# Performance work log

Measured on AMD Instinct MI355X. Metric: run time of the kernel, lower is better.

The kernel has to match this reference:

```python
import jax, jax.numpy as jnp
import numpy as np
from jax.ops import segment_sum

N_NODES = 50000
N_EDGES = 800000
IN_FEATS = 128
H_FEATS = 256
NUM_CLASSES = 16


def setup_inputs() -> dict:
    key = jax.random.key(0)
    k1, k2, k3, k4, k5 = jax.random.split(key, 5)
    in_feat = jax.random.normal(k1, (N_NODES, IN_FEATS), dtype=jnp.float32)
    src = jax.random.randint(k2, (N_EDGES,), 0, N_NODES, dtype=jnp.int32)
    dst = jax.random.randint(k3, (N_EDGES,), 0, N_NODES, dtype=jnp.int32)
    # Glorot-ish scaled params
    W_gc = jax.random.normal(k4, (IN_FEATS, H_FEATS), dtype=jnp.float32) / np.sqrt(IN_FEATS)
    b_gc = jnp.zeros((H_FEATS,), dtype=jnp.float32)
    W_fc = jax.random.normal(k5, (H_FEATS, NUM_CLASSES), dtype=jnp.float32) / np.sqrt(H_FEATS)
    b_fc = jnp.zeros((NUM_CLASSES,), dtype=jnp.float32)
    return {"in_feat": in_feat, "src": src, "dst": dst,
            "W_gc": W_gc, "b_gc": b_gc, "W_fc": W_fc, "b_fc": b_fc}


def reference(in_feat, src, dst, W_gc, b_gc, W_fc, b_fc):
    n = in_feat.shape[0]
    ones = jnp.ones_like(src, dtype=in_feat.dtype)
    # DGL GraphConv, norm='both': D_out^{-1/2} on source side, sum-aggregate,
    # D_in^{-1/2} on destination side. Degrees clamped to >= 1.
    deg_out = jnp.clip(segment_sum(ones, src, num_segments=n), 1.0)
    deg_in = jnp.clip(segment_sum(ones, dst, num_segments=n), 1.0)
    x = in_feat * jax.lax.rsqrt(deg_out)[:, None]            # [N, in]
    agg = segment_sum(x[src], dst, num_segments=n)           # [N, in] irregular gather+scatter
    agg = agg * jax.lax.rsqrt(deg_in)[:, None]
    # in_feats <= h_feats -> aggregate first, then project (DGL ordering)
    h = agg @ W_gc + b_gc                                    # [N, h]
    h = jax.nn.relu(h)
    logits = h @ W_fc + b_fc                                 # [N, num_classes]
    return jax.nn.sigmoid(logits)
```

## Files before the change

kernel.cpp:

```cpp
#include <hip/hip_runtime.h>
#include <hip/hip_bf16.h>

#define IN_F  128
#define H_F   256
#define NC    16
#define BM    64
#define CAP   64
#define PCAP  8192

typedef short bf16x8 __attribute__((ext_vector_type(8)));
typedef float f32x4  __attribute__((ext_vector_type(4)));

__device__ __forceinline__ unsigned short f2bf(float x) {
    union { float f; unsigned u; } v; v.f = x;
    unsigned r = v.u + 0x7FFF + ((v.u >> 16) & 1);
    return (unsigned short)(r >> 16);
}
__device__ __forceinline__ float bflo(unsigned x) {
    union { unsigned u; float f; } v; v.u = x << 16; return v.f;
}
__device__ __forceinline__ float bfhi(unsigned x) {
    union { unsigned u; float f; } v; v.u = x & 0xffff0000u; return v.f;
}

__global__ void gcn_zero(int* __restrict__ cur, unsigned* __restrict__ xb, int n) {
    int tid = threadIdx.x;
    cur[tid] = 0;
    cur[tid + 256] = 0;
    if (tid < 64) xb[(size_t)n * 64 + tid] = 0;
}

__global__ __launch_bounds__(256) void gcn_part(
    const int* __restrict__ src, const int* __restrict__ dst,
    int* __restrict__ curS, int* __restrict__ curD,
    unsigned short* __restrict__ srcP, unsigned* __restrict__ dstP,
    const float* __restrict__ W_gc, const float* __restrict__ W_fc,
    unsigned short* __restrict__ Wp, unsigned short* __restrict__ Wfp,
    const float* __restrict__ in_feat, unsigned* __restrict__ xb,
    int n_edges, int n_feat4, int nb_edge, int np) {
    __shared__ int cS[256], cD[256];
    int b0 = blockIdx.x, tid = threadIdx.x;
    if (b0 < nb_edge) {
        unsigned sv[16], dv[16];
        int ebase = b0 * 4096;
        #pragma unroll
        for (int r = 0; r < 16; ++r) {
            int e = ebase + r * 256 + tid;
            if (e < n_edges) { sv[r] = (unsigned)src[e]; dv[r] = (unsigned)dst[e]; }
            else { sv[r] = 0xFFFFFFFFu; dv[r] = 0xFFFFFFFFu; }
        }
        cS[tid] = 0; cD[tid] = 0;
        __syncthreads();
        #pragma unroll
        for (int r = 0; r < 16; ++r) {
            if (dv[r] != 0xFFFFFFFFu) {
                atomicAdd(&cS[sv[r] >> 8], 1);
                atomicAdd(&cD[dv[r] >> 8], 1);
            }
        }
        __syncthreads();
        if (tid < np) {
            int c = cS[tid];
            cS[tid] = c ? atomicAdd(&curS[tid], c) : 0;
            c = cD[tid];
            cD[tid] = c ? atomicAdd(&curD[tid], c) : 0;
        }
        __syncthreads();
        #pragma unroll
        for (int r = 0; r < 16; ++r) {
            if (dv[r] != 0xFFFFFFFFu) {
                unsigned s = sv[r], d = dv[r];
                int ps = atomicAdd(&cS[s >> 8], 1);
                if (ps < PCAP) srcP[(size_t)(s >> 8) * PCAP + ps] = (unsigned short)s;
                int pd = atomicAdd(&cD[d >> 8], 1);
                if (pd < PCAP) dstP[(size_t)(d >> 8) * PCAP + pd] =
                    ((d & 255u) << 16) | (s & 0xffffu);
            }
        }
        return;
    }
    int b = b0 - nb_edge;
    if (b < 128) {
        int g = b * 256 + tid;
        {
            int j = g & 7, l = (g >> 3) & 63, t = g >> 9;
            int kt = t & 3, ct = t >> 2;
            int k = kt * 32 + ((l >> 4) << 3) + j;
            int col = ct * 16 + (l & 15);
            Wp[g] = f2bf(W_gc[k * 256 + col]);
        }
        if (g < 4096) {
            int j = g & 7, l = (g >> 3) & 63, kt = g >> 9;
            int k = kt * 32 + ((l >> 4) << 3) + j;
            Wfp[g] = f2bf(W_fc[k * 16 + (l & 15)]);
        }
        return;
    }
    int idx = (b - 128) * 256 + tid;
    if (idx < n_feat4) {
        float4 v = ((const float4*)in_feat)[idx];
        uint2 o;
        o.x = (unsigned)f2bf(v.x) | ((unsigned)f2bf(v.y) << 16);
        o.y = (unsigned)f2bf(v.z) | ((unsigned)f2bf(v.w) << 16);
        ((uint2*)xb)[idx] = o;
    }
}

__global__ __launch_bounds__(256) void gcn_bucket(
    const unsigned short* __restrict__ srcP, const unsigned* __restrict__ dstP,
    const int* __restrict__ curS, const int* __restrict__ curD,
    int* __restrict__ cnt_out, int* __restrict__ cnt_in,
    unsigned short* __restrict__ esrc, unsigned* __restrict__ xb,
    int n, int np) {
    __shared__ unsigned hist[256];
    __shared__ float rr[256];
    __shared__ unsigned short bucket[256 * CAP];
    int p = blockIdx.x, tid = threadIdx.x;
    hist[tid] = 0;
    __syncthreads();
    if (p < np) {
        int cnt = curS[p]; if (cnt > PCAP) cnt = PCAP;
        const unsigned short* sp = srcP + (size_t)p * PCAP;
        for (int i = tid; i < cnt; i += 256)
            atomicAdd(&hist[sp[i] & 255], 1);
        __syncthreads();
        int node = p * 256 + tid;
        if (node < n) cnt_out[node] = (int)hist[tid];
        rr[tid] = rsqrtf(fmaxf((float)hist[tid], 1.0f));
        __syncthreads();
        for (int i = tid; i < 16384; i += 256) {
            int row = i >> 6, el = i & 63;
            int nd = p * 256 + row;
            if (nd < n) {
                unsigned v = xb[(size_t)nd * 64 + el];
                float r = rr[row];
                float lo = bflo(v) * r;
                float hi = bfhi(v) * r;
                xb[(size_t)nd * 64 + el] = (unsigned)f2bf(lo) | ((unsigned)f2bf(hi) << 16);
            }
        }
    } else {
        int pp = p - np;
        unsigned dummy2 = ((unsigned)n & 0xffffu) | (((unsigned)n & 0xffffu) << 16);
        unsigned* bu32 = (unsigned*)bucket;
        for (int i = tid; i < 8192; i += 256) bu32[i] = dummy2;
        int cnt = curD[pp]; if (cnt > PCAP) cnt = PCAP;
        const unsigned* dp = dstP + (size_t)pp * PCAP;
        __syncthreads();
        for (int i = tid; i < cnt; i += 256) {
            unsigned pair = dp[i];
            unsigned dl = pair >> 16;
            unsigned pos = atomicAdd(&hist[dl], 1);
            if (pos < CAP) bucket[(dl << 6) + pos] = (unsigned short)(pair & 0xffffu);
        }
        __syncthreads();
        unsigned* eb = (unsigned*)(esrc + ((size_t)pp << 14));
        const unsigned* bu = (const unsigned*)bucket;
        int maxrow = n - pp * 256;
        int words = (maxrow >= 256) ? 8192 : (maxrow > 0 ? maxrow * 32 : 0);
        for (int i = tid; i < words; i += 256) eb[i] = bu[i];
        int node = pp * 256 + tid;
        if (node < n) cnt_in[node] = (int)hist[tid];
    }
}

__global__ __launch_bounds__(256) void gcn_aggregate(
    const unsigned* __restrict__ xb, const unsigned short* __restrict__ esrc,
    const int* __restrict__ cnt_in, unsigned* __restrict__ aggb, int n) {
    int wave = (blockIdx.x * blockDim.x + threadIdx.x) >> 6;
    int lane = threadIdx.x & 63;
    if (wave >= n) return;
    int wv = __builtin_amdgcn_readfirstlane(wave);
    int cnt = cnt_in[wv];
    if (cnt > CAP) cnt = CAP;
    const unsigned short* es = esrc + ((size_t)wv << 6);
    const uint2* xb2 = (const uint2*)xb;
    int half = lane >> 5;
    int sub  = lane & 31;
    int hsh  = half * 16;
    float a0[8], a1[8], a2[8], a3[8];
    #pragma unroll
    for (int j = 0; j < 8; ++j) { a0[j] = 0.f; a1[j] = 0.f; a2[j] = 0.f; a3[j] = 0.f; }
    for (int i = 0; i < cnt; i += 16) {
        uint4 pa = *(const uint4*)(es + i);
        uint4 pb = *(const uint4*)(es + i + 8);
        unsigned wrd[8];
        wrd[0] = pa.x; wrd[1] = pa.y; wrd[2] = pa.z; wrd[3] = pa.w;
        wrd[4] = pb.x; wrd[5] = pb.y; wrd[6] = pb.z; wrd[7] = pb.w;
        #pragma unroll
        for (int j = 0; j < 8; ++j) {
            int s = (int)((wrd[j] >> hsh) & 0xffffu);
            uint2 v = xb2[(size_t)s * 32 + sub];
            a0[j] += bflo(v.x); a1[j] += bfhi(v.x);
            a2[j] += bflo(v.y); a3[j] += bfhi(v.y);
        }
    }
    float s0 = ((a0[0]+a0[1])+(a0[2]+a0[3]))+((a0[4]+a0[5])+(a0[6]+a0[7]));
    float s1 = ((a1[0]+a1[1])+(a1[2]+a1[3]))+((a1[4]+a1[5])+(a1[6]+a1[7]));
    float s2 = ((a2[0]+a2[1])+(a2[2]+a2[3]))+((a2[4]+a2[5])+(a2[6]+a2[7]));
    float s3 = ((a3[0]+a3[1])+(a3[2]+a3[3]))+((a3[4]+a3[5])+(a3[6]+a3[7]));
    s0 += __shfl_xor(s0, 32);
    s1 += __shfl_xor(s1, 32);
    s2 += __shfl_xor(s2, 32);
    s3 += __shfl_xor(s3, 32);
    if (half == 0) {
        float ri = rsqrtf(fmaxf((float)cnt, 1.0f));
        uint2 o;
        o.x = (unsigned)f2bf(s0 * ri) | ((unsigned)f2bf(s1 * ri) << 16);
        o.y = (unsigned)f2bf(s2 * ri) | ((unsigned)f2bf(s3 * ri) << 16);
        ((uint2*)aggb)[(size_t)wv * 32 + sub] = o;
    }
}

__global__ __launch_bounds__(256) void gcn_mlp(
    const unsigned* __restrict__ aggb, const unsigned short* __restrict__ Wp,
    const unsigned short* __restrict__ Wfp, const float* __restrict__ b_gc,
    const float* __restrict__ b_fc, float* __restrict__ out, int n) {
    extern __shared__ char smraw[];
    unsigned short* Wl  = (unsigned short*)smraw;
    unsigned short* Wfl = Wl + 32768;
    unsigned short* Al  = Wfl + 4096;
    unsigned short* Hl  = Al + 8192;
    float* bgl = (float*)(Hl + 16384);
    float* bfl = bgl + 256;

    int tid = threadIdx.x;
    int lane = tid & 63, w = tid >> 6;

    for (int i = tid; i < 4096; i += 256) ((float4*)Wl)[i]  = ((const float4*)Wp)[i];
    for (int i = tid; i < 512;  i += 256) ((float4*)Wfl)[i] = ((const float4*)Wfp)[i];
    bgl[tid] = b_gc[tid];
    if (tid < NC) bfl[tid] = b_fc[tid];

    int ntiles = (n + BM - 1) / BM;
    for (int tile = blockIdx.x; tile < ntiles; tile += gridDim.x) {
        __syncthreads();
        int row0 = tile * BM;
        for (int i = tid; i < 1024; i += 256) {
            int r = i >> 4, cb = i & 15;
            int node = row0 + r;
            float4 v = (node < n) ? ((const float4*)aggb)[(size_t)node * 16 + cb]
                                  : make_float4(0.f, 0.f, 0.f, 0.f);
            ((float4*)Al)[r * 16 + (cb ^ (r & 7))] = v;
        }
        __syncthreads();

        bf16x8 af[4];
        {
            int r = lane & 15;
            #pragma unroll
            for (int kt = 0; kt < 4; ++kt) {
                int cb = kt * 4 + (lane >> 4);
                af[kt] = *((const bf16x8*)Al + ((w * 16 + r) * 16 + (cb ^ (r & 7))));
            }
        }
        f32x4 acc[16];
        #pragma unroll
        for (int ct = 0; ct < 16; ++ct) {
            acc[ct] = (f32x4){0.f, 0.f, 0.f, 0.f};
            #pragma unroll
            for (int kt = 0; kt < 4; ++kt) {
                bf16x8 bfr = *((const bf16x8*)Wl + ((ct * 4 + kt) * 64 + lane));
                acc[ct] = __builtin_amdgcn_mfma_f32_16x16x32_bf16(af[kt], bfr, acc[ct], 0, 0, 0);
            }
        }
        #pragma unroll
        for (int ct = 0; ct < 16; ++ct) {
            int col = ct * 16 + (lane & 15);
            float bv = bgl[col];
            #pragma unroll
            for (int r4 = 0; r4 < 4; ++r4) {
                int r = ((lane >> 4) << 2) + r4;
                float hv = fmaxf(acc[ct][r4] + bv, 0.f);
                int cu = col >> 3;
                Hl[(w * 16 + r) * 256 + ((cu ^ (r & 7)) << 3) + (col & 7)] = f2bf(hv);
            }
        }
        f32x4 acc2 = (f32x4){0.f, 0.f, 0.f, 0.f};
        {
            int r = lane & 15;
            #pragma unroll
            for (int kt = 0; kt < 8; ++kt) {
                int cu = kt * 4 + (lane >> 4);
                bf16x8 a2 = *((const bf16x8*)Hl + ((w * 16 + r) * 32 + (cu ^ (r & 7))));
                bf16x8 b2 = *((const bf16x8*)Wfl + (kt * 64 + lane));
                acc2 = __builtin_amdgcn_mfma_f32_16x16x32_bf16(a2, b2, acc2, 0, 0, 0);
            }
        }
        int col = lane & 15;
        float bv = bfl[col];
        #pragma unroll
        for (int r4 = 0; r4 < 4; ++r4) {
            int row = row0 + w * 16 + ((lane >> 4) << 2) + r4;
            if (row < n) {
                float v = acc2[r4] + bv;
                out[(size_t)row * NC + col] = 1.f / (1.f + expf(-v));
            }
        }
    }
}

extern "C" void kernel_launch(void* const* d_in, const int* in_sizes, int n_in,
                              void* d_out, int out_size, void* d_ws, size_t ws_size,
                              hipStream_t stream) {
    const float* in_feat = (const float*)d_in[0];
    const int*   src     = (const int*)d_in[1];
    const int*   dst     = (const int*)d_in[2];
    const float* W_gc    = (const float*)d_in[3];
    const float* b_gc    = (const float*)d_in[4];
    const float* W_fc    = (const float*)d_in[5];
    const float* b_fc    = (const float*)d_in[6];
    float* out = (float*)d_out;

    int n_nodes = in_sizes[0] / IN_F;
    int n_edges = in_sizes[1];
    int np = (n_nodes + 255) >> 8;

    int* curS = (int*)d_ws;
    int* curD = curS + 256;
    int* cnt_out = curD + 256;
    int* cnt_in  = cnt_out + n_nodes;
    unsigned short* srcP = (unsigned short*)(cnt_in + n_nodes);
    unsigned* dstP = (unsigned*)(srcP + (size_t)np * PCAP);
    unsigned short* esrc = (unsigned short*)(dstP + (size_t)np * PCAP);
    unsigned short* Wp   = esrc + (size_t)np * 256 * CAP;
    unsigned short* Wfp  = Wp + 32768;
    unsigned* xb   = (unsigned*)(Wfp + 4096);
    unsigned* aggb = xb + (size_t)(n_nodes + 1) * 64;

    gcn_zero<<<1, 256, 0, stream>>>(curS, xb, n_nodes);

    {
        int n_feat4 = n_nodes * 32;
        int nb_edge = (n_edges + 4095) / 4096;
        int nb_conv = (n_feat4 + 255) / 256;
        gcn_part<<<nb_edge + 128 + nb_conv, 256, 0, stream>>>(
            src, dst, curS, curD, srcP, dstP, W_gc, W_fc, Wp, Wfp,
            in_feat, xb, n_edges, n_feat4, nb_edge, np);
    }
    gcn_bucket<<<2 * np, 256, 0, stream>>>(srcP, dstP, curS, curD,
                                           cnt_out, cnt_in, esrc, xb, n_nodes, np);
    {
        int blocks = (n_nodes + 3) / 4;
        gcn_aggregate<<<blocks, 256, 0, stream>>>(xb, esrc, cnt_in, aggb, n_nodes);
    }
    {
        size_t smem = 65536 + 8192 + 16384 + 32768 + 1024 + 64;
        hipFuncSetAttribute((const void*)gcn_mlp,
                            hipFuncAttributeMaxDynamicSharedMemorySize, (int)smem);
        gcn_mlp<<<256, 256, smem, stream>>>(aggb, Wp, Wfp, b_gc, b_fc, out, n_nodes);
    }
}
```

Before: 104.9 us.

## Split aggregation feature dimension across four blocks per node group

The gather-aggregate kernel now splits each node's 128-feature row into four quarters, each handled by a separate block, with the quarter index taken from the low bits of the block id. Each wave loads the edge list once and broadcasts source ids by shuffle, processing four edges per round with 16 lanes per edge on 4-byte loads. This gives four times as many waves and lanes per edge load, meant to raise memory-level parallelism and to even out load across nodes with different degrees. The cost is narrower per-lane loads, repeated edge-list and count reads across the four blocks, and less unrolling per wave.

```diff
diff --git a/kernel.cpp b/kernel.cpp
--- a/kernel.cpp
+++ b/kernel.cpp
@@ -167,48 +167,32 @@
 __global__ __launch_bounds__(256) void gcn_aggregate(
     const unsigned* __restrict__ xb, const unsigned short* __restrict__ esrc,
     const int* __restrict__ cnt_in, unsigned* __restrict__ aggb, int n) {
-    int wave = (blockIdx.x * blockDim.x + threadIdx.x) >> 6;
+    int b = blockIdx.x;
+    int slot = b & 7;
+    int q = slot & 3;
+    int g = (b >> 3) * 2 + (slot >> 2);
+    int node = g * 4 + (threadIdx.x >> 6);
     int lane = threadIdx.x & 63;
-    if (wave >= n) return;
-    int wv = __builtin_amdgcn_readfirstlane(wave);
-    int cnt = cnt_in[wv];
+    if (node >= n) return;
+    int nv = __builtin_amdgcn_readfirstlane(node);
+    int cnt = cnt_in[nv];
     if (cnt > CAP) cnt = CAP;
-    const unsigned short* es = esrc + ((size_t)wv << 6);
-    const uint2* xb2 = (const uint2*)xb;
-    int half = lane >> 5;
-    int sub  = lane & 31;
-    int hsh  = half * 16;
-    float a0[8], a1[8], a2[8], a3[8];
-    #pragma unroll
-    for (int j = 0; j < 8; ++j) { a0[j] = 0.f; a1[j] = 0.f; a2[j] = 0.f; a3[j] = 0.f; }
-    for (int i = 0; i < cnt; i += 16) {
-        uint4 pa = *(const uint4*)(es + i);
-        uint4 pb = *(const uint4*)(es + i + 8);
-        unsigned wrd[8];
-        wrd[0] = pa.x; wrd[1] = pa.y; wrd[2] = pa.z; wrd[3] = pa.w;
-        wrd[4] = pb.x; wrd[5] = pb.y; wrd[6] = pb.z; wrd[7] = pb.w;
-        #pragma unroll
-        for (int j = 0; j < 8; ++j) {
-            int s = (int)((wrd[j] >> hsh) & 0xffffu);
-            uint2 v = xb2[(size_t)s * 32 + sub];
-            a0[j] += bflo(v.x); a1[j] += bfhi(v.x);
-            a2[j] += bflo(v.y); a3[j] += bfhi(v.y);
-        }
-    }
-    float s0 = ((a0[0]+a0[1])+(a0[2]+a0[3]))+((a0[4]+a0[5])+(a0[6]+a0[7]));
-    float s1 = ((a1[0]+a1[1])+(a1[2]+a1[3]))+((a1[4]+a1[5])+(a1[6]+a1[7]));
-    float s2 = ((a2[0]+a2[1])+(a2[2]+a2[3]))+((a2[4]+a2[5])+(a2[6]+a2[7]));
-    float s3 = ((a3[0]+a3[1])+(a3[2]+a3[3]))+((a3[4]+a3[5])+(a3[6]+a3[7]));
-    s0 += __shfl_xor(s0, 32);
-    s1 += __shfl_xor(s1, 32);
-    s2 += __shfl_xor(s2, 32);
-    s3 += __shfl_xor(s3, 32);
-    if (half == 0) {
+    const unsigned short* es = esrc + ((size_t)nv << 6);
+    unsigned esv = (unsigned)es[lane];
+    int e4 = lane >> 4, f16 = lane & 15;
+    float acc0 = 0.f, acc1 = 0.f;
+    int rounds = (cnt + 3) >> 2;
+    for (int r = 0; r < rounds; ++r) {
+        unsigned s = (unsigned)__shfl((int)esv, r * 4 + e4);
+        unsigned v = xb[(size_t)s * 64 + q * 16 + f16];
+        acc0 += bflo(v); acc1 += bfhi(v);
+    }
+    acc0 += __shfl_xor(acc0, 16); acc0 += __shfl_xor(acc0, 32);
+    acc1 += __shfl_xor(acc1, 16); acc1 += __shfl_xor(acc1, 32);
+    if (e4 == 0) {
         float ri = rsqrtf(fmaxf((float)cnt, 1.0f));
-        uint2 o;
-        o.x = (unsigned)f2bf(s0 * ri) | ((unsigned)f2bf(s1 * ri) << 16);
-        o.y = (unsigned)f2bf(s2 * ri) | ((unsigned)f2bf(s3 * ri) << 16);
-        ((uint2*)aggb)[(size_t)wv * 32 + sub] = o;
+        aggb[(size_t)nv * 64 + q * 16 + f16] =
+            (unsigned)f2bf(acc0 * ri) | ((unsigned)f2bf(acc1 * ri) << 16);
     }
 }
 
@@ -341,7 +325,8 @@
     gcn_bucket<<<2 * np, 256, 0, stream>>>(srcP, dstP, curS, curD,
                                            cnt_out, cnt_in, esrc, xb, n_nodes, np);
     {
-        int blocks = (n_nodes + 3) / 4;
+        int ngroups = (n_nodes + 3) / 4;
+        int blocks = 8 * ((ngroups + 1) / 2);
         gcn_aggregate<<<blocks, 256, 0, stream>>>(xb, esrc, cnt_in, aggb, n_nodes);
     }
     {
```

Result: slower. 152.4 us (+45.3%).

## Sort per-node edge lists by source range and gather full rows per wave

Applied to the files above, without the earlier changes.

The bucket kernel now pads each node's edge row to avoid bank conflicts and counting-sorts the source indices into four coarse ranges (by the top two bits) before writing them out. The aggregation kernel drops the half-wave split: each lane loads one 32-bit word of the 256-byte row for eight neighbours per iteration, removing the cross-half shuffle. The goal is better cache locality on the gather and less reduction overhead, at the cost of extra serial per-thread sorting work and more shared memory in the bucket kernel.

```diff
diff --git a/kernel.cpp b/kernel.cpp
--- a/kernel.cpp
+++ b/kernel.cpp
@@ -7,6 +7,7 @@
 #define BM    64
 #define CAP   64
 #define PCAP  8192
+#define ROWP  66
 
 typedef short bf16x8 __attribute__((ext_vector_type(8)));
 typedef float f32x4  __attribute__((ext_vector_type(4)));
@@ -112,9 +113,11 @@
     int* __restrict__ cnt_out, int* __restrict__ cnt_in,
     unsigned short* __restrict__ esrc, unsigned* __restrict__ xb,
     int n, int np) {
-    __shared__ unsigned hist[256];
-    __shared__ float rr[256];
-    __shared__ unsigned short bucket[256 * CAP];
+    extern __shared__ char smem[];
+    unsigned* hist = (unsigned*)smem;
+    float* rr = (float*)(hist + 256);
+    unsigned short* bucket  = (unsigned short*)(rr + 256);
+    unsigned short* bucket2 = bucket + 256 * ROWP;
     int p = blockIdx.x, tid = threadIdx.x;
     hist[tid] = 0;
     __syncthreads();
@@ -142,8 +145,8 @@
     } else {
         int pp = p - np;
         unsigned dummy2 = ((unsigned)n & 0xffffu) | (((unsigned)n & 0xffffu) << 16);
-        unsigned* bu32 = (unsigned*)bucket;
-        for (int i = tid; i < 8192; i += 256) bu32[i] = dummy2;
+        unsigned* b2_32 = (unsigned*)bucket2;
+        for (int i = tid; i < 256 * (ROWP / 2); i += 256) b2_32[i] = dummy2;
         int cnt = curD[pp]; if (cnt > PCAP) cnt = PCAP;
         const unsigned* dp = dstP + (size_t)pp * PCAP;
         __syncthreads();
@@ -151,14 +154,35 @@
             unsigned pair = dp[i];
             unsigned dl = pair >> 16;
             unsigned pos = atomicAdd(&hist[dl], 1);
-            if (pos < CAP) bucket[(dl << 6) + pos] = (unsigned short)(pair & 0xffffu);
+            if (pos < CAP) bucket[dl * ROWP + pos] = (unsigned short)(pair & 0xffffu);
+        }
+        __syncthreads();
+        {
+            int c = (int)hist[tid]; if (c > CAP) c = CAP;
+            const unsigned short* row = bucket + tid * ROWP;
+            int c0 = 0, c1 = 0, c2 = 0, c3 = 0;
+            for (int i = 0; i < c; ++i) {
+                int k = row[i] >> 14;
+                c0 += (k == 0); c1 += (k == 1); c2 += (k == 2); c3 += (k == 3);
+            }
+            int o0 = 0, o1 = c0, o2 = c0 + c1, o3 = c0 + c1 + c2;
+            unsigned short* row2 = bucket2 + tid * ROWP;
+            for (int i = 0; i < c; ++i) {
+                unsigned short s = row[i];
+                int k = s >> 14;
+                int off = (k == 0) ? o0 : (k == 1) ? o1 : (k == 2) ? o2 : o3;
+                row2[off] = s;
+                o0 += (k == 0); o1 += (k == 1); o2 += (k == 2); o3 += (k == 3);
+            }
         }
         __syncthreads();
         unsigned* eb = (unsigned*)(esrc + ((size_t)pp << 14));
-        const unsigned* bu = (const unsigned*)bucket;
         int maxrow = n - pp * 256;
         int words = (maxrow >= 256) ? 8192 : (maxrow > 0 ? maxrow * 32 : 0);
-        for (int i = tid; i < words; i += 256) eb[i] = bu[i];
+        for (int i = tid; i < words; i += 256) {
+            int nd = i >> 5, j = i & 31;
+            eb[i] = b2_32[nd * (ROWP / 2) + j];
+        }
         int node = pp * 256 + tid;
         if (node < n) cnt_in[node] = (int)hist[tid];
     }
@@ -174,42 +198,37 @@
     int cnt = cnt_in[wv];
     if (cnt > CAP) cnt = CAP;
     const unsigned short* es = esrc + ((size_t)wv << 6);
-    const uint2* xb2 = (const uint2*)xb;
-    int half = lane >> 5;
-    int sub  = lane & 31;
-    int hsh  = half * 16;
-    float a0[8], a1[8], a2[8], a3[8];
+    float al[8], ah[8];
     #pragma unroll
-    for (int j = 0; j < 8; ++j) { a0[j] = 0.f; a1[j] = 0.f; a2[j] = 0.f; a3[j] = 0.f; }
-    for (int i = 0; i < cnt; i += 16) {
-        uint4 pa = *(const uint4*)(es + i);
-        uint4 pb = *(const uint4*)(es + i + 8);
-        unsigned wrd[8];
-        wrd[0] = pa.x; wrd[1] = pa.y; wrd[2] = pa.z; wrd[3] = pa.w;
-        wrd[4] = pb.x; wrd[5] = pb.y; wrd[6] = pb.z; wrd[7] = pb.w;
-        #pragma unroll
-        for (int j = 0; j < 8; ++j) {
-            int s = (int)((wrd[j] >> hsh) & 0xffffu);
-            uint2 v = xb2[(size_t)s * 32 + sub];
-            a0[j] += bflo(v.x); a1[j] += bfhi(v.x);
-            a2[j] += bflo(v.y); a3[j] += bfhi(v.y);
-        }
-    }
-    float s0 = ((a0[0]+a0[1])+(a0[2]+a0[3]))+((a0[4]+a0[5])+(a0[6]+a0[7]));
-    float s1 = ((a1[0]+a1[1])+(a1[2]+a1[3]))+((a1[4]+a1[5])+(a1[6]+a1[7]));
-    float s2 = ((a2[0]+a2[1])+(a2[2]+a2[3]))+((a2[4]+a2[5])+(a2[6]+a2[7]));
-    float s3 = ((a3[0]+a3[1])+(a3[2]+a3[3]))+((a3[4]+a3[5])+(a3[6]+a3[7]));
-    s0 += __shfl_xor(s0, 32);
-    s1 += __shfl_xor(s1, 32);
-    s2 += __shfl_xor(s2, 32);
-    s3 += __shfl_xor(s3, 32);
-    if (half == 0) {
-        float ri = rsqrtf(fmaxf((float)cnt, 1.0f));
-        uint2 o;
-        o.x = (unsigned)f2bf(s0 * ri) | ((unsigned)f2bf(s1 * ri) << 16);
-        o.y = (unsigned)f2bf(s2 * ri) | ((unsigned)f2bf(s3 * ri) << 16);
-        ((uint2*)aggb)[(size_t)wv * 32 + sub] = o;
-    }
+    for (int u = 0; u < 8; ++u) { al[u] = 0.f; ah[u] = 0.f; }
+    for (int i = 0; i < cnt; i += 8) {
+        uint4 w = *(const uint4*)(es + i);
+        int s0 = w.x & 0xffff, s1 = w.x >> 16;
+        int s2 = w.y & 0xffff, s3 = w.y >> 16;
+        int s4 = w.z & 0xffff, s5 = w.z >> 16;
+        int s6 = w.w & 0xffff, s7 = w.w >> 16;
+        unsigned v0 = xb[(size_t)s0 * 64 + lane];
+        unsigned v1 = xb[(size_t)s1 * 64 + lane];
+        unsigned v2 = xb[(size_t)s2 * 64 + lane];
+        unsigned v3 = xb[(size_t)s3 * 64 + lane];
+        unsigned v4 = xb[(size_t)s4 * 64 + lane];
+        unsigned v5 = xb[(size_t)s5 * 64 + lane];
+        unsigned v6 = xb[(size_t)s6 * 64 + lane];
+        unsigned v7 = xb[(size_t)s7 * 64 + lane];
+        al[0] += bflo(v0); ah[0] += bfhi(v0);
+        al[1] += bflo(v1); ah[1] += bfhi(v1);
+        al[2] += bflo(v2); ah[2] += bfhi(v2);
+        al[3] += bflo(v3); ah[3] += bfhi(v3);
+        al[4] += bflo(v4); ah[4] += bfhi(v4);
+        al[5] += bflo(v5); ah[5] += bfhi(v5);
+        al[6] += bflo(v6); ah[6] += bfhi(v6);
+        al[7] += bflo(v7); ah[7] += bfhi(v7);
+    }
+    float sl = ((al[0]+al[1])+(al[2]+al[3]))+((al[4]+al[5])+(al[6]+al[7]));
+    float sh = ((ah[0]+ah[1])+(ah[2]+ah[3]))+((ah[4]+ah[5])+(ah[6]+ah[7]));
+    float ri = rsqrtf(fmaxf((float)cnt, 1.0f));
+    aggb[(size_t)wv * 64 + lane] =
+        (unsigned)f2bf(sl * ri) | ((unsigned)f2bf(sh * ri) << 16);
 }
 
 __global__ __launch_bounds__(256) void gcn_mlp(
@@ -338,8 +357,13 @@
             src, dst, curS, curD, srcP, dstP, W_gc, W_fc, Wp, Wfp,
             in_feat, xb, n_edges, n_feat4, nb_edge, np);
     }
-    gcn_bucket<<<2 * np, 256, 0, stream>>>(srcP, dstP, curS, curD,
-                                           cnt_out, cnt_in, esrc, xb, n_nodes, np);
+    {
+        size_t smem = 256 * 4 + 256 * 4 + 2 * (size_t)256 * ROWP * 2;
+        hipFuncSetAttribute((const void*)gcn_bucket,
+                            hipFuncAttributeMaxDynamicSharedMemorySize, (int)smem);
+        gcn_bucket<<<2 * np, 256, smem, stream>>>(srcP, dstP, curS, curD,
+                                                  cnt_out, cnt_in, esrc, xb, n_nodes, np);
+    }
     {
         int blocks = (n_nodes + 3) / 4;
         gcn_aggregate<<<blocks, 256, 0, stream>>>(xb, esrc, cnt_in, aggb, n_nodes);
```

New measurement: 105.5 us. Within noise of the previous version (+0.6%).
